# Kernel tuning notes

Measured on AMD Instinct MI355X. Metric: run time of the kernel, lower is better.

Reference implementation:

```python
import jax, jax.numpy as jnp
import numpy as np

BATCH = 1024
SEQ = 80
VOCAB = 50000
EMB = 512
UNITS = 512


def setup_inputs() -> dict:
    key = jax.random.key(0)
    ks = jax.random.split(key, 10)
    s_in = 1.0 / np.sqrt(EMB)
    s_h = 1.0 / np.sqrt(UNITS)
    return {
        "inputs": jax.random.randint(ks[0], (BATCH, SEQ), 0, VOCAB, dtype=jnp.int64),
        "emb": jax.random.normal(ks[1], (VOCAB, EMB), dtype=jnp.float32) * 0.05,
        "W0x": jax.random.normal(ks[2], (EMB, UNITS), dtype=jnp.float32) * s_in,
        "W0h": jax.random.normal(ks[3], (UNITS, UNITS), dtype=jnp.float32) * s_h,
        "b0": jnp.zeros((UNITS,), dtype=jnp.float32),
        "W1x": jax.random.normal(ks[4], (UNITS, UNITS), dtype=jnp.float32) * s_h,
        "W1h": jax.random.normal(ks[5], (UNITS, UNITS), dtype=jnp.float32) * s_h,
        "b1": jnp.zeros((UNITS,), dtype=jnp.float32),
        "Wout": jax.random.normal(ks[6], (UNITS, 1), dtype=jnp.float32) * s_h,
        "bout": jnp.zeros((1,), dtype=jnp.float32),
    }


def reference(inputs, emb, W0x, W0h, b0, W1x, W1h, b1, Wout, bout):
    # Embedding lookup: [B, T, E]
    x = emb[inputs]
    # Time-major for scan: [T, B, E]
    xs = jnp.transpose(x, (1, 0, 2))

    h0 = jnp.zeros((inputs.shape[0], W0h.shape[0]), dtype=emb.dtype)
    h1 = jnp.zeros((inputs.shape[0], W1h.shape[0]), dtype=emb.dtype)

    def step(carry, x_t):
        h0, h1 = carry
        # SimpleRNNCell 0: tanh(x@Wx + h@Wh + b)  (dropout inactive at inference)
        h0 = jnp.tanh(x_t @ W0x + h0 @ W0h + b0)
        # SimpleRNNCell 1 stacked on cell 0's output
        h1 = jnp.tanh(h0 @ W1x + h1 @ W1h + b1)
        return (h0, h1), None

    (h0, h1), _ = jax.lax.scan(step, (h0, h1), xs)
    # Dense(1) on last-step hidden of layer 1, then sigmoid -> [B, 1]
    prob = jax.nn.sigmoid(h1 @ Wout + bout)
    return prob
```

## Files before the change

### kernel.cpp

```cpp
#include <hip/hip_runtime.h>
#include <hip/hip_bf16.h>
#include <math.h>

#define BATCH   1024
#define SEQ     80
#define EMB     512
#define UNITS   512
#define NBG     64
#define NCG     4
#define ROWS    16
#define COLS    128
#define THREADS 512
#define LDW     1544

#define H0_OFF   (2u * 1024 * 1024)
#define H1_OFF   (4u * 1024 * 1024)
#define FLAG_OFF (6u * 1024 * 1024)

typedef __attribute__((ext_vector_type(8))) short          bf16x8;
typedef __attribute__((ext_vector_type(8))) unsigned short u16x8;
typedef __attribute__((ext_vector_type(4))) float          f32x4;

__device__ inline unsigned short f2bf(float f) {
    __hip_bfloat16 h = __float2bfloat16(f);
    return *reinterpret_cast<unsigned short*>(&h);
}
__device__ inline float bf2f(unsigned short u) {
    unsigned int x = ((unsigned int)u) << 16;
    return __uint_as_float(x);
}
__device__ inline float tanh_fast(float x) {
    float e = __expf(2.f * x);
    return 1.f - 2.f / (e + 1.f);
}

__global__ __launch_bounds__(256) void pack_weights(
    const float* __restrict__ W0x, const float* __restrict__ W0h,
    const float* __restrict__ W1x, const float* __restrict__ W1h,
    unsigned short* __restrict__ wpack)
{
    int g    = blockIdx.x * 4 + (threadIdx.x >> 6);
    int lane = threadIdx.x & 63;
    int p    = g >> 10;
    int cg   = (g >> 8) & 3;
    int w    = (g >> 5) & 7;
    int k0   = g & 31;
    int n    = cg * COLS + w * 16 + (lane & 15);
    int kb   = k0 * 32 + (lane >> 4) * 8;
    const float* Wx = p ? W1x : W0x;
    const float* Wh = p ? W1h : W0h;

    u16x8 v;
#pragma unroll
    for (int j = 0; j < 8; ++j) {
        int k = kb + j;
        float f = (k < 512) ? Wx[(size_t)k * UNITS + n]
                            : Wh[(size_t)(k - 512) * UNITS + n];
        v[j] = f2bf(f);
    }
    *(u16x8*)(wpack + (size_t)g * 512 + lane * 8) = v;
}

#define RUN_PHASE(ACC, KBASE, WB)                                              \
    do {                                                                       \
        const unsigned short* a_lds = hcat + abase + (KBASE);                  \
        bf16x8 Bf[8];                                                          \
        _Pragma("unroll")                                                      \
        for (int i = 0; i < 8; ++i)                                            \
            Bf[i] = *(const bf16x8*)((WB) + (size_t)i * 512);                  \
        _Pragma("unroll")                                                      \
        for (int k0 = 0; k0 < 32; ++k0) {                                      \
            bf16x8 a = *(const bf16x8*)(a_lds + k0 * 32);                      \
            bf16x8 b = Bf[k0 & 7];                                             \
            if (k0 + 8 < 32)                                                   \
                Bf[k0 & 7] = *(const bf16x8*)((WB) + (size_t)(k0 + 8) * 512);  \
            ACC = __builtin_amdgcn_mfma_f32_16x16x32_bf16(a, b, ACC, 0, 0, 0); \
        }                                                                      \
    } while (0)

__global__ __launch_bounds__(THREADS, 1) void rnn_ex_kernel(
    const int*   __restrict__ inputs,
    const float* __restrict__ emb,
    const float* __restrict__ b0,
    const float* __restrict__ b1,
    const unsigned short* __restrict__ wpack,
    unsigned short* __restrict__ h0buf,
    unsigned short* __restrict__ h1buf,
    int* __restrict__ flag0,
    int* __restrict__ flag1,
    const float* __restrict__ Wout,
    const float* __restrict__ bout,
    float*       __restrict__ out)
{
    __shared__ unsigned short hcat[ROWS * LDW];

    const int tid   = threadIdx.x;
    const int w     = tid >> 6;
    const int lane  = tid & 63;
    const int quad  = lane >> 4;
    const int l15   = lane & 15;
    const int cg    = blockIdx.x >> 6;
    const int bg    = blockIdx.x & 63;
    const int rbase = bg * ROWS;

    for (int i = tid; i < ROWS * 1024; i += THREADS) {
        int r = i >> 10, c = i & 1023;
        hcat[r * LDW + 512 + c] = 0;
    }

    const int xr = tid >> 5;
    const int xc = (tid & 31) * 16;

    {
        int idx = inputs[(rbase + xr) * SEQ + 0];
        const float4* ep = (const float4*)(emb + (size_t)idx * EMB + xc);
        float4 p0 = ep[0], p1 = ep[1], p2 = ep[2], p3 = ep[3];
        u16x8 v0, v1;
        v0[0]=f2bf(p0.x); v0[1]=f2bf(p0.y); v0[2]=f2bf(p0.z); v0[3]=f2bf(p0.w);
        v0[4]=f2bf(p1.x); v0[5]=f2bf(p1.y); v0[6]=f2bf(p1.z); v0[7]=f2bf(p1.w);
        v1[0]=f2bf(p2.x); v1[1]=f2bf(p2.y); v1[2]=f2bf(p2.z); v1[3]=f2bf(p2.w);
        v1[4]=f2bf(p3.x); v1[5]=f2bf(p3.y); v1[6]=f2bf(p3.z); v1[7]=f2bf(p3.w);
        *(u16x8*)(hcat + xr * LDW + xc)     = v0;
        *(u16x8*)(hcat + xr * LDW + xc + 8) = v1;
    }
    __syncthreads();

    const int   mycol = cg * COLS + w * 16 + l15;
    const float bias0 = b0[mycol];
    const float bias1 = b1[mycol];

    const unsigned short* wb0 = wpack + ((size_t)(cg * 256 + w * 32)) * 512 + lane * 8;
    const unsigned short* wb1 = wb0 + (size_t)1024 * 512;

    const int abase = l15 * LDW + quad * 8;
    const int fl    = bg * NCG;

    for (int t = 0; t < SEQ; ++t) {
        const int par = t & 1;
        const int tgt = t + 1;

        int tn = (t + 1 < SEQ) ? t + 1 : t;
        int idx = inputs[(rbase + xr) * SEQ + tn];
        const float4* ep = (const float4*)(emb + (size_t)idx * EMB + xc);
        float4 p0 = ep[0], p1 = ep[1], p2 = ep[2], p3 = ep[3];

        f32x4 acc = {bias0, bias0, bias0, bias0};
        RUN_PHASE(acc, 0, wb0);
        {
            unsigned short* dst = h0buf +
                ((size_t)par * BATCH + rbase + quad * 4) * UNITS + mycol;
#pragma unroll
            for (int i = 0; i < 4; ++i)
                __hip_atomic_store(dst + (size_t)i * UNITS,
                                   f2bf(tanh_fast(acc[i])),
                                   __ATOMIC_RELAXED, __HIP_MEMORY_SCOPE_AGENT);
        }
        __syncthreads();
        if (tid == 0)
            __hip_atomic_store(&flag0[fl + cg], tgt,
                               __ATOMIC_RELEASE, __HIP_MEMORY_SCOPE_AGENT);
        if (tid < NCG)
            while (__hip_atomic_load(&flag0[fl + tid],
                                     __ATOMIC_RELAXED, __HIP_MEMORY_SCOPE_AGENT) < tgt)
                __builtin_amdgcn_s_sleep(1);
        __asm__ volatile("" ::: "memory");
        __syncthreads();
        {
            const unsigned long long* src = (const unsigned long long*)
                (h0buf + ((size_t)par * BATCH + rbase) * UNITS);
            int base = (xr * 512 + xc) >> 2;
            unsigned long long q0 = __hip_atomic_load(src + base + 0, __ATOMIC_RELAXED, __HIP_MEMORY_SCOPE_AGENT);
            unsigned long long q1 = __hip_atomic_load(src + base + 1, __ATOMIC_RELAXED, __HIP_MEMORY_SCOPE_AGENT);
            unsigned long long q2 = __hip_atomic_load(src + base + 2, __ATOMIC_RELAXED, __HIP_MEMORY_SCOPE_AGENT);
            unsigned long long q3 = __hip_atomic_load(src + base + 3, __ATOMIC_RELAXED, __HIP_MEMORY_SCOPE_AGENT);
            unsigned long long* d = (unsigned long long*)&hcat[xr * LDW + 512 + xc];
            d[0] = q0; d[1] = q1; d[2] = q2; d[3] = q3;

            u16x8 v0, v1;
            v0[0]=f2bf(p0.x); v0[1]=f2bf(p0.y); v0[2]=f2bf(p0.z); v0[3]=f2bf(p0.w);
            v0[4]=f2bf(p1.x); v0[5]=f2bf(p1.y); v0[6]=f2bf(p1.z); v0[7]=f2bf(p1.w);
            v1[0]=f2bf(p2.x); v1[1]=f2bf(p2.y); v1[2]=f2bf(p2.z); v1[3]=f2bf(p2.w);
            v1[4]=f2bf(p3.x); v1[5]=f2bf(p3.y); v1[6]=f2bf(p3.z); v1[7]=f2bf(p3.w);
            *(u16x8*)(hcat + xr * LDW + xc)     = v0;
            *(u16x8*)(hcat + xr * LDW + xc + 8) = v1;
        }
        __syncthreads();

        f32x4 acc2 = {bias1, bias1, bias1, bias1};
        RUN_PHASE(acc2, 512, wb1);
        {
            unsigned short* dst = h1buf +
                ((size_t)par * BATCH + rbase + quad * 4) * UNITS + mycol;
#pragma unroll
            for (int i = 0; i < 4; ++i)
                __hip_atomic_store(dst + (size_t)i * UNITS,
                                   f2bf(tanh_fast(acc2[i])),
                                   __ATOMIC_RELAXED, __HIP_MEMORY_SCOPE_AGENT);
        }
        __syncthreads();
        if (tid == 0)
            __hip_atomic_store(&flag1[fl + cg], tgt,
                               __ATOMIC_RELEASE, __HIP_MEMORY_SCOPE_AGENT);
        if (tid < NCG)
            while (__hip_atomic_load(&flag1[fl + tid],
                                     __ATOMIC_RELAXED, __HIP_MEMORY_SCOPE_AGENT) < tgt)
                __builtin_amdgcn_s_sleep(1);
        __asm__ volatile("" ::: "memory");
        __syncthreads();
        {
            const unsigned long long* src = (const unsigned long long*)
                (h1buf + ((size_t)par * BATCH + rbase) * UNITS);
            int base = (xr * 512 + xc) >> 2;
            unsigned long long q0 = __hip_atomic_load(src + base + 0, __ATOMIC_RELAXED, __HIP_MEMORY_SCOPE_AGENT);
            unsigned long long q1 = __hip_atomic_load(src + base + 1, __ATOMIC_RELAXED, __HIP_MEMORY_SCOPE_AGENT);
            unsigned long long q2 = __hip_atomic_load(src + base + 2, __ATOMIC_RELAXED, __HIP_MEMORY_SCOPE_AGENT);
            unsigned long long q3 = __hip_atomic_load(src + base + 3, __ATOMIC_RELAXED, __HIP_MEMORY_SCOPE_AGENT);
            unsigned long long* d = (unsigned long long*)&hcat[xr * LDW + 1024 + xc];
            d[0] = q0; d[1] = q1; d[2] = q2; d[3] = q3;
        }
    }
    __syncthreads();

    if (cg == 0) {
#pragma unroll
        for (int rr = 0; rr < 2; ++rr) {
            int r = w * 2 + rr;
            float s = 0.f;
#pragma unroll
            for (int j = 0; j < 8; ++j) {
                int c = lane + 64 * j;
                s += bf2f(hcat[r * LDW + 1024 + c]) * Wout[c];
            }
#pragma unroll
            for (int off = 32; off > 0; off >>= 1) s += __shfl_down(s, off);
            if (lane == 0) {
                float z = s + bout[0];
                out[rbase + r] = 1.f / (1.f + __expf(-z));
            }
        }
    }
}

extern "C" void kernel_launch(void* const* d_in, const int* in_sizes, int n_in,
                              void* d_out, int out_size, void* d_ws, size_t ws_size,
                              hipStream_t stream) {
    const int*   inputs = (const int*)d_in[0];
    const float* emb    = (const float*)d_in[1];
    const float* W0x    = (const float*)d_in[2];
    const float* W0h    = (const float*)d_in[3];
    const float* b0     = (const float*)d_in[4];
    const float* W1x    = (const float*)d_in[5];
    const float* W1h    = (const float*)d_in[6];
    const float* b1     = (const float*)d_in[7];
    const float* Wout   = (const float*)d_in[8];
    const float* bout   = (const float*)d_in[9];
    float*       out    = (float*)d_out;

    unsigned short* wpack = (unsigned short*)d_ws;
    unsigned short* h0buf = (unsigned short*)((char*)d_ws + H0_OFF);
    unsigned short* h1buf = (unsigned short*)((char*)d_ws + H1_OFF);
    int* flag0 = (int*)((char*)d_ws + FLAG_OFF);
    int* flag1 = flag0 + 256;

    hipMemsetAsync((char*)d_ws + FLAG_OFF, 0, 2048, stream);
    pack_weights<<<512, 256, 0, stream>>>(W0x, W0h, W1x, W1h, wpack);
    rnn_ex_kernel<<<NBG * NCG, THREADS, 0, stream>>>(
        inputs, emb, b0, b1, wpack, h0buf, h1buf, flag0, flag1,
        Wout, bout, out);
}
```

Baseline: 1.137 ms.

## Retile RNN blocks to 32 rows, swizzle LDS, overlap GEMMs with flag waits

Each block now covers 32 batch rows and 64 columns with 256 threads, so every wave runs two MFMA accumulators that share one weight fragment. The padded LDS layout is replaced by an XOR-swizzled layout of 1024 elements per row. Independent work is moved in front of the cross-block flag waits: the h1-recurrent half of layer 1 and the next step's layer-0 GEMM both run while waiting. The aim is to hide the inter-block synchronisation latency and to reuse loaded weights. The cost is more registers per thread and a more complex schedule in which the order of hcat reads and writes must stay correct.

```diff
diff --git a/kernel.cpp b/kernel.cpp
--- a/kernel.cpp
+++ b/kernel.cpp
@@ -6,12 +6,11 @@
 #define SEQ     80
 #define EMB     512
 #define UNITS   512
-#define NBG     64
-#define NCG     4
-#define ROWS    16
-#define COLS    128
-#define THREADS 512
-#define LDW     1544
+#define NBG     32
+#define NCG     8
+#define ROWS    32
+#define COLS    64
+#define THREADS 256
 
 #define H0_OFF   (2u * 1024 * 1024)
 #define H1_OFF   (4u * 1024 * 1024)
@@ -42,8 +41,8 @@
     int g    = blockIdx.x * 4 + (threadIdx.x >> 6);
     int lane = threadIdx.x & 63;
     int p    = g >> 10;
-    int cg   = (g >> 8) & 3;
-    int w    = (g >> 5) & 7;
+    int cg   = (g >> 7) & 7;
+    int w    = (g >> 5) & 3;
     int k0   = g & 31;
     int n    = cg * COLS + w * 16 + (lane & 15);
     int kb   = k0 * 32 + (lane >> 4) * 8;
@@ -61,22 +60,29 @@
     *(u16x8*)(wpack + (size_t)g * 512 + lane * 8) = v;
 }
 
-#define RUN_PHASE(ACC, KBASE, WB)                                              \
-    do {                                                                       \
-        const unsigned short* a_lds = hcat + abase + (KBASE);                  \
-        bf16x8 Bf[8];                                                          \
-        _Pragma("unroll")                                                      \
-        for (int i = 0; i < 8; ++i)                                            \
-            Bf[i] = *(const bf16x8*)((WB) + (size_t)i * 512);                  \
-        _Pragma("unroll")                                                      \
-        for (int k0 = 0; k0 < 32; ++k0) {                                      \
-            bf16x8 a = *(const bf16x8*)(a_lds + k0 * 32);                      \
-            bf16x8 b = Bf[k0 & 7];                                             \
-            if (k0 + 8 < 32)                                                   \
-                Bf[k0 & 7] = *(const bf16x8*)((WB) + (size_t)(k0 + 8) * 512);  \
-            ACC = __builtin_amdgcn_mfma_f32_16x16x32_bf16(a, b, ACC, 0, 0, 0); \
-        }                                                                      \
-    } while (0)
+template<int NK, int GBASE>
+__device__ __forceinline__ void run_k(
+    f32x4& acc0, f32x4& acc1,
+    const unsigned short* __restrict__ wb,
+    const unsigned short* hcat, int l15, int quad, int sw)
+{
+    bf16x8 Bf[8];
+    constexpr int PRE = (NK < 8) ? NK : 8;
+#pragma unroll
+    for (int i = 0; i < PRE; ++i)
+        Bf[i] = *(const bf16x8*)(wb + (size_t)i * 512);
+#pragma unroll
+    for (int i = 0; i < NK; ++i) {
+        int g0 = ((GBASE + i * 4 + quad) ^ sw) * 8;
+        bf16x8 a0 = *(const bf16x8*)(hcat + l15 * 1024 + g0);
+        bf16x8 a1 = *(const bf16x8*)(hcat + (16 + l15) * 1024 + g0);
+        bf16x8 b  = Bf[i & 7];
+        if (i + 8 < NK)
+            Bf[i & 7] = *(const bf16x8*)(wb + (size_t)(i + 8) * 512);
+        acc0 = __builtin_amdgcn_mfma_f32_16x16x32_bf16(a0, b, acc0, 0, 0, 0);
+        acc1 = __builtin_amdgcn_mfma_f32_16x16x32_bf16(a1, b, acc1, 0, 0, 0);
+    }
+}
 
 __global__ __launch_bounds__(THREADS, 1) void rnn_ex_kernel(
     const int*   __restrict__ inputs,
@@ -92,36 +98,39 @@
     const float* __restrict__ bout,
     float*       __restrict__ out)
 {
-    __shared__ unsigned short hcat[ROWS * LDW];
+    __shared__ unsigned short hcat[ROWS * 1024];
 
     const int tid   = threadIdx.x;
     const int w     = tid >> 6;
     const int lane  = tid & 63;
     const int quad  = lane >> 4;
     const int l15   = lane & 15;
-    const int cg    = blockIdx.x >> 6;
-    const int bg    = blockIdx.x & 63;
+    const int sw    = l15 & 7;
+    const int cg    = blockIdx.x >> 5;
+    const int bg    = blockIdx.x & 31;
     const int rbase = bg * ROWS;
 
-    for (int i = tid; i < ROWS * 1024; i += THREADS) {
-        int r = i >> 10, c = i & 1023;
-        hcat[r * LDW + 512 + c] = 0;
-    }
-
-    const int xr = tid >> 5;
-    const int xc = (tid & 31) * 16;
+    for (int i = tid; i < ROWS * 512; i += THREADS) {
+        int r = i >> 9, c = i & 511;
+        hcat[r * 1024 + 512 + c] = 0;
+    }
+
+    const int xrow = tid >> 3;
+    const int xl8  = tid & 7;
 
     {
-        int idx = inputs[(rbase + xr) * SEQ + 0];
-        const float4* ep = (const float4*)(emb + (size_t)idx * EMB + xc);
-        float4 p0 = ep[0], p1 = ep[1], p2 = ep[2], p3 = ep[3];
-        u16x8 v0, v1;
-        v0[0]=f2bf(p0.x); v0[1]=f2bf(p0.y); v0[2]=f2bf(p0.z); v0[3]=f2bf(p0.w);
-        v0[4]=f2bf(p1.x); v0[5]=f2bf(p1.y); v0[6]=f2bf(p1.z); v0[7]=f2bf(p1.w);
-        v1[0]=f2bf(p2.x); v1[1]=f2bf(p2.y); v1[2]=f2bf(p2.z); v1[3]=f2bf(p2.w);
-        v1[4]=f2bf(p3.x); v1[5]=f2bf(p3.y); v1[6]=f2bf(p3.z); v1[7]=f2bf(p3.w);
-        *(u16x8*)(hcat + xr * LDW + xc)     = v0;
-        *(u16x8*)(hcat + xr * LDW + xc + 8) = v1;
+        int idx = inputs[(rbase + xrow) * SEQ + 0];
+        const float* ep = emb + (size_t)idx * EMB;
+#pragma unroll
+        for (int i = 0; i < 8; ++i) {
+            int c8 = i * 8 + xl8;
+            float4 fa = *(const float4*)(ep + c8 * 8);
+            float4 fb = *(const float4*)(ep + c8 * 8 + 4);
+            u16x8 v;
+            v[0]=f2bf(fa.x); v[1]=f2bf(fa.y); v[2]=f2bf(fa.z); v[3]=f2bf(fa.w);
+            v[4]=f2bf(fb.x); v[5]=f2bf(fb.y); v[6]=f2bf(fb.z); v[7]=f2bf(fb.w);
+            *(u16x8*)(hcat + xrow * 1024 + ((c8 ^ (xrow & 7)) * 8)) = v;
+        }
     }
     __syncthreads();
 
@@ -129,107 +138,143 @@
     const float bias0 = b0[mycol];
     const float bias1 = b1[mycol];
 
-    const unsigned short* wb0 = wpack + ((size_t)(cg * 256 + w * 32)) * 512 + lane * 8;
+    const unsigned short* wb0 = wpack + ((size_t)(cg * 4 + w) * 32) * 512 + lane * 8;
     const unsigned short* wb1 = wb0 + (size_t)1024 * 512;
-
-    const int abase = l15 * LDW + quad * 8;
-    const int fl    = bg * NCG;
+    const int fl = bg * NCG;
+
+    f32x4 acc0  = {bias0, bias0, bias0, bias0};
+    f32x4 acc0b = acc0;
+    run_k<32, 0>(acc0, acc0b, wb0, hcat, l15, quad, sw);
 
     for (int t = 0; t < SEQ; ++t) {
         const int par = t & 1;
         const int tgt = t + 1;
 
-        int tn = (t + 1 < SEQ) ? t + 1 : t;
-        int idx = inputs[(rbase + xr) * SEQ + tn];
-        const float4* ep = (const float4*)(emb + (size_t)idx * EMB + xc);
-        float4 p0 = ep[0], p1 = ep[1], p2 = ep[2], p3 = ep[3];
-
-        f32x4 acc = {bias0, bias0, bias0, bias0};
-        RUN_PHASE(acc, 0, wb0);
         {
             unsigned short* dst = h0buf +
                 ((size_t)par * BATCH + rbase + quad * 4) * UNITS + mycol;
 #pragma unroll
-            for (int i = 0; i < 4; ++i)
+            for (int i = 0; i < 4; ++i) {
                 __hip_atomic_store(dst + (size_t)i * UNITS,
-                                   f2bf(tanh_fast(acc[i])),
-                                   __ATOMIC_RELAXED, __HIP_MEMORY_SCOPE_AGENT);
-        }
+                    f2bf(tanh_fast(acc0[i])), __ATOMIC_RELAXED, __HIP_MEMORY_SCOPE_AGENT);
+                __hip_atomic_store(dst + (size_t)(16 + i) * UNITS,
+                    f2bf(tanh_fast(acc0b[i])), __ATOMIC_RELAXED, __HIP_MEMORY_SCOPE_AGENT);
+            }
+        }
+        int tn  = (t + 1 < SEQ) ? t + 1 : t;
+        int idx = inputs[(rbase + xrow) * SEQ + tn];
         __syncthreads();
         if (tid == 0)
             __hip_atomic_store(&flag0[fl + cg], tgt,
                                __ATOMIC_RELEASE, __HIP_MEMORY_SCOPE_AGENT);
+
+        const float* ep = emb + (size_t)idx * EMB;
+        float4 xf[16];
+#pragma unroll
+        for (int i = 0; i < 8; ++i) {
+            int c8 = i * 8 + xl8;
+            xf[2 * i]     = *(const float4*)(ep + c8 * 8);
+            xf[2 * i + 1] = *(const float4*)(ep + c8 * 8 + 4);
+        }
+
+        f32x4 acc2  = {bias1, bias1, bias1, bias1};
+        f32x4 acc2b = acc2;
+        if (t > 0)
+            run_k<16, 0>(acc2, acc2b, wb1 + (size_t)16 * 512, hcat, l15, quad, sw);
+
         if (tid < NCG)
             while (__hip_atomic_load(&flag0[fl + tid],
                                      __ATOMIC_RELAXED, __HIP_MEMORY_SCOPE_AGENT) < tgt)
                 __builtin_amdgcn_s_sleep(1);
         __asm__ volatile("" ::: "memory");
         __syncthreads();
+
         {
             const unsigned long long* src = (const unsigned long long*)
                 (h0buf + ((size_t)par * BATCH + rbase) * UNITS);
-            int base = (xr * 512 + xc) >> 2;
-            unsigned long long q0 = __hip_atomic_load(src + base + 0, __ATOMIC_RELAXED, __HIP_MEMORY_SCOPE_AGENT);
-            unsigned long long q1 = __hip_atomic_load(src + base + 1, __ATOMIC_RELAXED, __HIP_MEMORY_SCOPE_AGENT);
-            unsigned long long q2 = __hip_atomic_load(src + base + 2, __ATOMIC_RELAXED, __HIP_MEMORY_SCOPE_AGENT);
-            unsigned long long q3 = __hip_atomic_load(src + base + 3, __ATOMIC_RELAXED, __HIP_MEMORY_SCOPE_AGENT);
-            unsigned long long* d = (unsigned long long*)&hcat[xr * LDW + 512 + xc];
-            d[0] = q0; d[1] = q1; d[2] = q2; d[3] = q3;
-
-            u16x8 v0, v1;
-            v0[0]=f2bf(p0.x); v0[1]=f2bf(p0.y); v0[2]=f2bf(p0.z); v0[3]=f2bf(p0.w);
-            v0[4]=f2bf(p1.x); v0[5]=f2bf(p1.y); v0[6]=f2bf(p1.z); v0[7]=f2bf(p1.w);
-            v1[0]=f2bf(p2.x); v1[1]=f2bf(p2.y); v1[2]=f2bf(p2.z); v1[3]=f2bf(p2.w);
-            v1[4]=f2bf(p3.x); v1[5]=f2bf(p3.y); v1[6]=f2bf(p3.z); v1[7]=f2bf(p3.w);
-            *(u16x8*)(hcat + xr * LDW + xc)     = v0;
-            *(u16x8*)(hcat + xr * LDW + xc + 8) = v1;
-        }
-        __syncthreads();
-
-        f32x4 acc2 = {bias1, bias1, bias1, bias1};
-        RUN_PHASE(acc2, 512, wb1);
+#pragma unroll
+            for (int j = 0; j < 8; ++j) {
+                int G = j * 256 + tid;
+                int r = G >> 6, c8 = G & 63;
+                unsigned long long q0 = __hip_atomic_load(src + (size_t)G * 2,
+                    __ATOMIC_RELAXED, __HIP_MEMORY_SCOPE_AGENT);
+                unsigned long long q1 = __hip_atomic_load(src + (size_t)G * 2 + 1,
+                    __ATOMIC_RELAXED, __HIP_MEMORY_SCOPE_AGENT);
+                int off = r * 1024 + ((64 + c8) ^ (r & 7)) * 8;
+                *(unsigned long long*)(hcat + off)     = q0;
+                *(unsigned long long*)(hcat + off + 4) = q1;
+            }
+#pragma unroll
+            for (int i = 0; i < 8; ++i) {
+                int c8 = i * 8 + xl8;
+                float4 fa = xf[2 * i], fb = xf[2 * i + 1];
+                u16x8 v;
+                v[0]=f2bf(fa.x); v[1]=f2bf(fa.y); v[2]=f2bf(fa.z); v[3]=f2bf(fa.w);
+                v[4]=f2bf(fb.x); v[5]=f2bf(fb.y); v[6]=f2bf(fb.z); v[7]=f2bf(fb.w);
+                *(u16x8*)(hcat + xrow * 1024 + ((c8 ^ (xrow & 7)) * 8)) = v;
+            }
+        }
+        __syncthreads();
+
+        run_k<16, 64>(acc2, acc2b, wb1, hcat, l15, quad, sw);
+
         {
             unsigned short* dst = h1buf +
                 ((size_t)par * BATCH + rbase + quad * 4) * UNITS + mycol;
 #pragma unroll
-            for (int i = 0; i < 4; ++i)
+            for (int i = 0; i < 4; ++i) {
                 __hip_atomic_store(dst + (size_t)i * UNITS,
-                                   f2bf(tanh_fast(acc2[i])),
-                                   __ATOMIC_RELAXED, __HIP_MEMORY_SCOPE_AGENT);
+                    f2bf(tanh_fast(acc2[i])), __ATOMIC_RELAXED, __HIP_MEMORY_SCOPE_AGENT);
+                __hip_atomic_store(dst + (size_t)(16 + i) * UNITS,
+                    f2bf(tanh_fast(acc2b[i])), __ATOMIC_RELAXED, __HIP_MEMORY_SCOPE_AGENT);
+            }
         }
         __syncthreads();
         if (tid == 0)
             __hip_atomic_store(&flag1[fl + cg], tgt,
                                __ATOMIC_RELEASE, __HIP_MEMORY_SCOPE_AGENT);
+
+        acc0 = (f32x4){bias0, bias0, bias0, bias0};
+        acc0b = acc0;
+        if (t + 1 < SEQ)
+            run_k<32, 0>(acc0, acc0b, wb0, hcat, l15, quad, sw);
+
         if (tid < NCG)
             while (__hip_atomic_load(&flag1[fl + tid],
                                      __ATOMIC_RELAXED, __HIP_MEMORY_SCOPE_AGENT) < tgt)
                 __builtin_amdgcn_s_sleep(1);
         __asm__ volatile("" ::: "memory");
         __syncthreads();
+
         {
             const unsigned long long* src = (const unsigned long long*)
                 (h1buf + ((size_t)par * BATCH + rbase) * UNITS);
-            int base = (xr * 512 + xc) >> 2;
-            unsigned long long q0 = __hip_atomic_load(src + base + 0, __ATOMIC_RELAXED, __HIP_MEMORY_SCOPE_AGENT);
-            unsigned long long q1 = __hip_atomic_load(src + base + 1, __ATOMIC_RELAXED, __HIP_MEMORY_SCOPE_AGENT);
-            unsigned long long q2 = __hip_atomic_load(src + base + 2, __ATOMIC_RELAXED, __HIP_MEMORY_SCOPE_AGENT);
-            unsigned long long q3 = __hip_atomic_load(src + base + 3, __ATOMIC_RELAXED, __HIP_MEMORY_SCOPE_AGENT);
-            unsigned long long* d = (unsigned long long*)&hcat[xr * LDW + 1024 + xc];
-            d[0] = q0; d[1] = q1; d[2] = q2; d[3] = q3;
+#pragma unroll
+            for (int j = 0; j < 8; ++j) {
+                int G = j * 256 + tid;
+                int r = G >> 6, c8 = G & 63;
+                unsigned long long q0 = __hip_atomic_load(src + (size_t)G * 2,
+                    __ATOMIC_RELAXED, __HIP_MEMORY_SCOPE_AGENT);
+                unsigned long long q1 = __hip_atomic_load(src + (size_t)G * 2 + 1,
+                    __ATOMIC_RELAXED, __HIP_MEMORY_SCOPE_AGENT);
+                int off = r * 1024 + ((c8 ^ (r & 7)) * 8);
+                *(unsigned long long*)(hcat + off)     = q0;
+                *(unsigned long long*)(hcat + off + 4) = q1;
+            }
         }
     }
     __syncthreads();
 
     if (cg == 0) {
 #pragma unroll
-        for (int rr = 0; rr < 2; ++rr) {
-            int r = w * 2 + rr;
+        for (int rr = 0; rr < 8; ++rr) {
+            int r = w * 8 + rr;
             float s = 0.f;
 #pragma unroll
             for (int j = 0; j < 8; ++j) {
-                int c = lane + 64 * j;
-                s += bf2f(hcat[r * LDW + 1024 + c]) * Wout[c];
+                int c  = lane + 64 * j;
+                int c8 = c >> 3, ci = c & 7;
+                s += bf2f(hcat[r * 1024 + ((c8 ^ (r & 7)) * 8) + ci]) * Wout[c];
             }
 #pragma unroll
             for (int off = 32; off > 0; off >>= 1) s += __shfl_down(s, off);
```

After: 1.510 ms. 1.33x slower.
